# Kernel optimization log

Hardware: AMD Instinct MI355X
Metric: run time of the kernel (lower is better)

Reference implementation:

```python
import jax, jax.numpy as jnp
import numpy as np

B, H, S, D = 2, 16, 2048, 64


def setup_inputs() -> dict:
    key = jax.random.key(0)
    kq, kk, kv = jax.random.split(key, 3)
    queries = jax.random.normal(kq, (B, H, S, D), dtype=jnp.float32)
    keys = jax.random.normal(kk, (B, H, S, D), dtype=jnp.float32)
    values = jax.random.normal(kv, (B, H, S, D), dtype=jnp.float32)
    # causal mask: True = attend, False = masked (matches masked_fill(mask == 0, -inf))
    mask = jnp.tril(jnp.ones((S, S), dtype=bool))[None, None, :, :]
    return {"queries": queries, "keys": keys, "values": values, "mask": mask}


def reference(queries, keys, values, mask):
    d_k = queries.shape[-1]
    scale = 1.0 / jnp.sqrt(jnp.asarray(d_k, dtype=queries.dtype))
    # scores: [B,H,S,S]
    scores = jnp.einsum("bhqd,bhkd->bhqk", queries, keys) * scale
    scores = jnp.where(mask, scores, -jnp.inf)
    attention = jax.nn.softmax(scores, axis=-1)
    # dropout p=0.0 (eval-mode reference) -> identity
    return jnp.einsum("bhqk,bhkd->bhqd", attention, values)
```

## Files before the change

kernel.cpp:

```cpp
#include <hip/hip_runtime.h>
#include <hip/hip_bf16.h>

#define S_LEN 2048
#define D_DIM 64
#define KVB   64
#define QS    (0.125f * 1.44269504088896341f)

using f32x4  = __attribute__((ext_vector_type(4))) float;
using bf16x8 = __attribute__((ext_vector_type(8))) short;

__device__ __forceinline__ unsigned short f2bf(float f) {
    return __builtin_bit_cast(unsigned short, __float2bfloat16(f));
}
__device__ __forceinline__ unsigned pk2bf(float lo, float hi) {
    return (unsigned)f2bf(lo) | ((unsigned)f2bf(hi) << 16);
}
__device__ __forceinline__ int swz(int r, int c) {
    return (r * 64 + c) ^ ((r & 7) << 3);
}

template<int C>
__device__ __forceinline__ float dppf(float x) {
    return __builtin_bit_cast(float,
        __builtin_amdgcn_mov_dpp(__builtin_bit_cast(int, x), C, 0xf, 0xf, true));
}
__device__ __forceinline__ float red16_max(float v) {
    v = fmaxf(v, dppf<0xB1>(v));
    v = fmaxf(v, dppf<0x4E>(v));
    v = fmaxf(v, dppf<0x141>(v));
    v = fmaxf(v, dppf<0x140>(v));
    return v;
}
__device__ __forceinline__ float red16_sum(float v) {
    v += dppf<0xB1>(v);
    v += dppf<0x4E>(v);
    v += dppf<0x141>(v);
    v += dppf<0x140>(v);
    return v;
}

__global__ __launch_bounds__(256, 4)
void attn_fwd(const float* __restrict__ Qg, const float* __restrict__ Kg,
              const float* __restrict__ Vg, float* __restrict__ Og) {
    __shared__ __align__(16) unsigned short lds[20480];

    const int wg = blockIdx.x;
    const int x  = wg & 7;
    const int s  = (wg >> 3) & 31;
    const int r  = wg >> 8;
    const int bh = x * 4 + r;
    const int q  = (r & 1) ? (31 - s) : s;

    const int tid  = threadIdx.x;
    const int wid  = tid >> 6;
    const int lane = tid & 63;
    const int lo   = lane & 15;
    const int hi   = lane >> 4;

    const size_t boff = (size_t)bh * (S_LEN * D_DIM);
    const float* Qp = Qg + boff;
    const float* Kp = Kg + boff;
    const float* Vp = Vg + boff;
    float*       Op = Og + boff;

    const int qrow0 = q * 64 + wid * 16;

    bf16x8 qf[2];
    #pragma unroll
    for (int kc = 0; kc < 2; ++kc) {
        const float* src = Qp + (size_t)(qrow0 + lo) * D_DIM + kc * 32 + hi * 8;
        f32x4 a = *(const f32x4*)src;
        f32x4 b = *(const f32x4*)(src + 4);
        union { bf16x8 v; unsigned u[4]; } fr;
        fr.u[0] = pk2bf(a[0] * QS, a[1] * QS);
        fr.u[1] = pk2bf(a[2] * QS, a[3] * QS);
        fr.u[2] = pk2bf(b[0] * QS, b[1] * QS);
        fr.u[3] = pk2bf(b[2] * QS, b[3] * QS);
        qf[kc] = fr.v;
    }

    float mrow[4], lrow[4];
    f32x4 oacc[4];
    #pragma unroll
    for (int rr = 0; rr < 4; ++rr) { mrow[rr] = -INFINITY; lrow[rr] = 0.f; }
    #pragma unroll
    for (int dn = 0; dn < 4; ++dn) oacc[dn] = f32x4{0.f, 0.f, 0.f, 0.f};

    const int kr    = tid >> 2;
    const int kcb   = (tid & 3) << 4;
    const int vr    = (tid & 31) << 1;
    const int vcb   = (tid >> 5) << 3;
    const int pbase = 16384 + (wid << 10);

    const int T = q + 1;
    f32x4 kst[4], vst[4];

    {
        const float* ks = Kp + (size_t)kr * D_DIM + kcb;
        kst[0] = *(const f32x4*)ks;       kst[1] = *(const f32x4*)(ks + 4);
        kst[2] = *(const f32x4*)(ks + 8); kst[3] = *(const f32x4*)(ks + 12);
        const float* vs = Vp + (size_t)vr * D_DIM + vcb;
        vst[0] = *(const f32x4*)vs;           vst[1] = *(const f32x4*)(vs + 4);
        vst[2] = *(const f32x4*)(vs + D_DIM); vst[3] = *(const f32x4*)(vs + D_DIM + 4);
        union { uint4 w4; unsigned u[4]; } w;
        w.u[0] = pk2bf(kst[0][0], kst[0][1]); w.u[1] = pk2bf(kst[0][2], kst[0][3]);
        w.u[2] = pk2bf(kst[1][0], kst[1][1]); w.u[3] = pk2bf(kst[1][2], kst[1][3]);
        *(uint4*)&lds[swz(kr, kcb)] = w.w4;
        w.u[0] = pk2bf(kst[2][0], kst[2][1]); w.u[1] = pk2bf(kst[2][2], kst[2][3]);
        w.u[2] = pk2bf(kst[3][0], kst[3][1]); w.u[3] = pk2bf(kst[3][2], kst[3][3]);
        *(uint4*)&lds[swz(kr, kcb + 8)] = w.w4;
        #pragma unroll
        for (int c = 0; c < 8; ++c) {
            unsigned pv = pk2bf(vst[c >> 2][c & 3], vst[2 + (c >> 2)][c & 3]);
            *(unsigned*)&lds[4096 + swz(vcb + c, vr)] = pv;
        }
    }
    __syncthreads();

    for (int t = 0; t < T; ++t) {
        const int kA = (t & 1) << 13;
        const int vA = kA + 4096;
        const bool pf = (t + 1 < T);

        if (pf) {
            const int nb = (t + 1) * KVB;
            const float* ks = Kp + (size_t)(nb + kr) * D_DIM + kcb;
            kst[0] = *(const f32x4*)ks;       kst[1] = *(const f32x4*)(ks + 4);
            kst[2] = *(const f32x4*)(ks + 8); kst[3] = *(const f32x4*)(ks + 12);
            const float* vs = Vp + (size_t)(nb + vr) * D_DIM + vcb;
            vst[0] = *(const f32x4*)vs;           vst[1] = *(const f32x4*)(vs + 4);
            vst[2] = *(const f32x4*)(vs + D_DIM); vst[3] = *(const f32x4*)(vs + D_DIM + 4);
        }

        f32x4 sc[4];
        __builtin_amdgcn_s_setprio(1);
        #pragma unroll
        for (int nt = 0; nt < 4; ++nt) {
            f32x4 acc = f32x4{0.f, 0.f, 0.f, 0.f};
            #pragma unroll
            for (int kc = 0; kc < 2; ++kc) {
                bf16x8 kf = *(const bf16x8*)&lds[kA + swz(nt * 16 + lo, kc * 32 + hi * 8)];
                acc = __builtin_amdgcn_mfma_f32_16x16x32_bf16(qf[kc], kf, acc, 0, 0, 0);
            }
            sc[nt] = acc;
        }
        __builtin_amdgcn_s_setprio(0);
        if (t == q) {
            const int kb = t * KVB;
            #pragma unroll
            for (int nt = 0; nt < 4; ++nt)
                #pragma unroll
                for (int rr = 0; rr < 4; ++rr)
                    if (kb + nt * 16 + lo > qrow0 + hi * 4 + rr) sc[nt][rr] = -INFINITY;
        }
        float pm[4];
        #pragma unroll
        for (int rr = 0; rr < 4; ++rr)
            pm[rr] = red16_max(fmaxf(fmaxf(sc[0][rr], sc[1][rr]), fmaxf(sc[2][rr], sc[3][rr])));

        bool resc = false;
        #pragma unroll
        for (int rr = 0; rr < 4; ++rr) resc |= (pm[rr] > mrow[rr] + 8.f);
        if (__any(resc)) {
            #pragma unroll
            for (int rr = 0; rr < 4; ++rr) {
                const float mn = fmaxf(mrow[rr], pm[rr]);
                const float al = __builtin_amdgcn_exp2f(mrow[rr] - mn);
                mrow[rr] = mn;
                lrow[rr] *= al;
                #pragma unroll
                for (int dn = 0; dn < 4; ++dn) oacc[dn][rr] *= al;
            }
        }
        float rs[4] = {0.f, 0.f, 0.f, 0.f};
        #pragma unroll
        for (int nt = 0; nt < 4; ++nt)
            #pragma unroll
            for (int rr = 0; rr < 4; ++rr) {
                float p = __builtin_amdgcn_exp2f(sc[nt][rr] - mrow[rr]);
                rs[rr] += p;
                lds[pbase + swz(hi * 4 + rr, nt * 16 + lo)] = f2bf(p);
            }
        #pragma unroll
        for (int rr = 0; rr < 4; ++rr) lrow[rr] += red16_sum(rs[rr]);

        __builtin_amdgcn_s_setprio(1);
        #pragma unroll
        for (int dn = 0; dn < 4; ++dn)
            #pragma unroll
            for (int kc = 0; kc < 2; ++kc) {
                bf16x8 pfr = *(const bf16x8*)&lds[pbase + swz(lo, kc * 32 + hi * 8)];
                bf16x8 vfr = *(const bf16x8*)&lds[vA + swz(dn * 16 + lo, kc * 32 + hi * 8)];
                oacc[dn] = __builtin_amdgcn_mfma_f32_16x16x32_bf16(pfr, vfr, oacc[dn], 0, 0, 0);
            }
        __builtin_amdgcn_s_setprio(0);

        if (pf) {
            const int nA = ((t + 1) & 1) << 13;
            union { uint4 w4; unsigned u[4]; } w;
            w.u[0] = pk2bf(kst[0][0], kst[0][1]); w.u[1] = pk2bf(kst[0][2], kst[0][3]);
            w.u[2] = pk2bf(kst[1][0], kst[1][1]); w.u[3] = pk2bf(kst[1][2], kst[1][3]);
            *(uint4*)&lds[nA + swz(kr, kcb)] = w.w4;
            w.u[0] = pk2bf(kst[2][0], kst[2][1]); w.u[1] = pk2bf(kst[2][2], kst[2][3]);
            w.u[2] = pk2bf(kst[3][0], kst[3][1]); w.u[3] = pk2bf(kst[3][2], kst[3][3]);
            *(uint4*)&lds[nA + swz(kr, kcb + 8)] = w.w4;
            #pragma unroll
            for (int c = 0; c < 8; ++c) {
                unsigned pv = pk2bf(vst[c >> 2][c & 3], vst[2 + (c >> 2)][c & 3]);
                *(unsigned*)&lds[nA + 4096 + swz(vcb + c, vr)] = pv;
            }
        }
        __syncthreads();
    }

    #pragma unroll
    for (int rr = 0; rr < 4; ++rr) {
        const float inv = 1.0f / lrow[rr];
        #pragma unroll
        for (int dn = 0; dn < 4; ++dn)
            Op[(size_t)(qrow0 + hi * 4 + rr) * D_DIM + dn * 16 + lo] = oacc[dn][rr] * inv;
    }
}

extern "C" void kernel_launch(void* const* d_in, const int* in_sizes, int n_in,
                              void* d_out, int out_size, void* d_ws, size_t ws_size,
                              hipStream_t stream) {
    const float* Q = (const float*)d_in[0];
    const float* K = (const float*)d_in[1];
    const float* V = (const float*)d_in[2];
    float* O = (float*)d_out;
    attn_fwd<<<dim3(32 * 32), dim3(256), 0, stream>>>(Q, K, V, O);
}
```

Baseline: 166.2 us.

## Pre-convert K/V to swizzled bf16 workspace and stage via global_load_lds

Adds two prep kernels that convert K to bf16 and V to transposed bf16, each already in the swizzled LDS tile layout, and write them to the workspace. The attention kernel then copies each tile straight from global memory into LDS with global_load_lds, so the per-iteration fp32 loads, conversions and LDS stores are gone, along with about half the bytes read per tile. The cost is two extra launches and an extra round trip of K/V through memory. The old kernel is kept as a fallback when the workspace is too small.

Result: faster. 151.0 us (-9.1%).

```diff
diff --git a/kernel.cpp b/kernel.cpp
--- a/kernel.cpp
+++ b/kernel.cpp
@@ -39,9 +39,57 @@
     return v;
 }
 
+typedef const __attribute__((address_space(1))) unsigned short* gas_p;
+typedef __attribute__((address_space(3))) unsigned short*       las_p;
+__device__ __forceinline__ void stage16(const unsigned short* g, unsigned short* l) {
+    __builtin_amdgcn_global_load_lds((gas_p)g, (las_p)l, 16, 0, 0);
+}
+
+__global__ __launch_bounds__(256)
+void prep_k(const float* __restrict__ Kg, unsigned short* __restrict__ wsK) {
+    const int base = (blockIdx.x * 256 + threadIdx.x) * 8;
+    const int bh   = base >> 17;
+    const int rem  = base & 131071;
+    const int r    = rem >> 6;
+    const int c0   = rem & 63;
+    f32x4 a = *(const f32x4*)(Kg + base);
+    f32x4 b = *(const f32x4*)(Kg + base + 4);
+    union { uint4 w4; unsigned u[4]; } w;
+    w.u[0] = pk2bf(a[0], a[1]); w.u[1] = pk2bf(a[2], a[3]);
+    w.u[2] = pk2bf(b[0], b[1]); w.u[3] = pk2bf(b[2], b[3]);
+    *(uint4*)&wsK[bh * 131072 + (r >> 6) * 4096 + swz(r & 63, c0)] = w.w4;
+}
+
+__global__ __launch_bounds__(256)
+void prep_v(const float* __restrict__ Vg, unsigned short* __restrict__ wsV) {
+    __shared__ float ldsF[64 * 68];
+    const int bh  = blockIdx.x >> 5;
+    const int t   = blockIdx.x & 31;
+    const int tid = threadIdx.x;
+    const int kvr = tid >> 2;
+    const int c0  = (tid & 3) << 4;
+    const float* src = Vg + (size_t)bh * 131072 + (size_t)(t * 64 + kvr) * 64 + c0;
+    #pragma unroll
+    for (int j = 0; j < 4; ++j)
+        *(f32x4*)&ldsF[kvr * 68 + c0 + j * 4] = *(const f32x4*)(src + j * 4);
+    __syncthreads();
+    #pragma unroll
+    for (int i = 0; i < 2; ++i) {
+        const int d   = tid & 63;
+        const int kv0 = ((tid >> 6) << 3) + (i << 5);
+        float p[8];
+        #pragma unroll
+        for (int j = 0; j < 8; ++j) p[j] = ldsF[(kv0 + j) * 68 + d];
+        union { uint4 w4; unsigned u[4]; } w;
+        w.u[0] = pk2bf(p[0], p[1]); w.u[1] = pk2bf(p[2], p[3]);
+        w.u[2] = pk2bf(p[4], p[5]); w.u[3] = pk2bf(p[6], p[7]);
+        *(uint4*)&wsV[bh * 131072 + t * 4096 + swz(d, kv0)] = w.w4;
+    }
+}
+
 __global__ __launch_bounds__(256, 4)
-void attn_fwd(const float* __restrict__ Qg, const float* __restrict__ Kg,
-              const float* __restrict__ Vg, float* __restrict__ Og) {
+void attn_fast(const float* __restrict__ Qg, const unsigned short* __restrict__ wsK,
+               const unsigned short* __restrict__ wsV, float* __restrict__ Og) {
     __shared__ __align__(16) unsigned short lds[20480];
 
     const int wg = blockIdx.x;
@@ -57,11 +105,10 @@
     const int lo   = lane & 15;
     const int hi   = lane >> 4;
 
-    const size_t boff = (size_t)bh * (S_LEN * D_DIM);
-    const float* Qp = Qg + boff;
-    const float* Kp = Kg + boff;
-    const float* Vp = Vg + boff;
-    float*       Op = Og + boff;
+    const float* Qp = Qg + (size_t)bh * (S_LEN * D_DIM);
+    float*       Op = Og + (size_t)bh * (S_LEN * D_DIM);
+    const unsigned short* kws = wsK + (size_t)bh * 131072;
+    const unsigned short* vws = wsV + (size_t)bh * 131072;
 
     const int qrow0 = q * 64 + wid * 16;
 
@@ -86,15 +133,155 @@
     #pragma unroll
     for (int dn = 0; dn < 4; ++dn) oacc[dn] = f32x4{0.f, 0.f, 0.f, 0.f};
 
+    const int pbase = 16384 + (wid << 10);
+    const int T = q + 1;
+
+    #pragma unroll
+    for (int j = 0; j < 2; ++j) {
+        const int so = (wid * 2 + j) * 512;
+        stage16(kws + so + lane * 8, &lds[so]);
+        stage16(vws + so + lane * 8, &lds[4096 + so]);
+    }
+    __syncthreads();
+
+    for (int t = 0; t < T; ++t) {
+        const int kA = (t & 1) << 13;
+        const int vA = kA + 4096;
+        const bool pf = (t + 1 < T);
+
+        if (pf) {
+            const int nA = ((t + 1) & 1) << 13;
+            const int tb = (t + 1) * 4096;
+            #pragma unroll
+            for (int j = 0; j < 2; ++j) {
+                const int so = (wid * 2 + j) * 512;
+                stage16(kws + tb + so + lane * 8, &lds[nA + so]);
+                stage16(vws + tb + so + lane * 8, &lds[nA + 4096 + so]);
+            }
+        }
+
+        f32x4 sc[4];
+        __builtin_amdgcn_s_setprio(1);
+        #pragma unroll
+        for (int nt = 0; nt < 4; ++nt) {
+            f32x4 acc = f32x4{0.f, 0.f, 0.f, 0.f};
+            #pragma unroll
+            for (int kc = 0; kc < 2; ++kc) {
+                bf16x8 kf = *(const bf16x8*)&lds[kA + swz(nt * 16 + lo, kc * 32 + hi * 8)];
+                acc = __builtin_amdgcn_mfma_f32_16x16x32_bf16(qf[kc], kf, acc, 0, 0, 0);
+            }
+            sc[nt] = acc;
+        }
+        __builtin_amdgcn_s_setprio(0);
+        if (t == q) {
+            const int kb = t * KVB;
+            #pragma unroll
+            for (int nt = 0; nt < 4; ++nt)
+                #pragma unroll
+                for (int rr = 0; rr < 4; ++rr)
+                    if (kb + nt * 16 + lo > qrow0 + hi * 4 + rr) sc[nt][rr] = -INFINITY;
+        }
+        float pm[4];
+        #pragma unroll
+        for (int rr = 0; rr < 4; ++rr)
+            pm[rr] = red16_max(fmaxf(fmaxf(sc[0][rr], sc[1][rr]), fmaxf(sc[2][rr], sc[3][rr])));
+
+        bool resc = false;
+        #pragma unroll
+        for (int rr = 0; rr < 4; ++rr) resc |= (pm[rr] > mrow[rr] + 8.f);
+        if (__any(resc)) {
+            #pragma unroll
+            for (int rr = 0; rr < 4; ++rr) {
+                const float mn = fmaxf(mrow[rr], pm[rr]);
+                const float al = __builtin_amdgcn_exp2f(mrow[rr] - mn);
+                mrow[rr] = mn;
+                lrow[rr] *= al;
+                #pragma unroll
+                for (int dn = 0; dn < 4; ++dn) oacc[dn][rr] *= al;
+            }
+        }
+        float rs[4] = {0.f, 0.f, 0.f, 0.f};
+        #pragma unroll
+        for (int nt = 0; nt < 4; ++nt)
+            #pragma unroll
+            for (int rr = 0; rr < 4; ++rr) {
+                float p = __builtin_amdgcn_exp2f(sc[nt][rr] - mrow[rr]);
+                rs[rr] += p;
+                lds[pbase + swz(hi * 4 + rr, nt * 16 + lo)] = f2bf(p);
+            }
+        #pragma unroll
+        for (int rr = 0; rr < 4; ++rr) lrow[rr] += red16_sum(rs[rr]);
+
+        __builtin_amdgcn_s_setprio(1);
+        #pragma unroll
+        for (int dn = 0; dn < 4; ++dn)
+            #pragma unroll
+            for (int kc = 0; kc < 2; ++kc) {
+                bf16x8 pfr = *(const bf16x8*)&lds[pbase + swz(lo, kc * 32 + hi * 8)];
+                bf16x8 vfr = *(const bf16x8*)&lds[vA + swz(dn * 16 + lo, kc * 32 + hi * 8)];
+                oacc[dn] = __builtin_amdgcn_mfma_f32_16x16x32_bf16(pfr, vfr, oacc[dn], 0, 0, 0);
+            }
+        __builtin_amdgcn_s_setprio(0);
+
+        __syncthreads();
+    }
+
+    #pragma unroll
+    for (int rr = 0; rr < 4; ++rr) {
+        const float inv = 1.0f / lrow[rr];
+        #pragma unroll
+        for (int dn = 0; dn < 4; ++dn)
+            Op[(size_t)(qrow0 + hi * 4 + rr) * D_DIM + dn * 16 + lo] = oacc[dn][rr] * inv;
+    }
+}
+
+__global__ __launch_bounds__(256, 4)
+void attn_fb(const float* __restrict__ Qg, const float* __restrict__ Kg,
+             const float* __restrict__ Vg, float* __restrict__ Og) {
+    __shared__ __align__(16) unsigned short lds[20480];
+    const int wg = blockIdx.x;
+    const int x  = wg & 7;
+    const int s  = (wg >> 3) & 31;
+    const int r  = wg >> 8;
+    const int bh = x * 4 + r;
+    const int q  = (r & 1) ? (31 - s) : s;
+    const int tid  = threadIdx.x;
+    const int wid  = tid >> 6;
+    const int lane = tid & 63;
+    const int lo   = lane & 15;
+    const int hi   = lane >> 4;
+    const size_t boff = (size_t)bh * (S_LEN * D_DIM);
+    const float* Qp = Qg + boff;
+    const float* Kp = Kg + boff;
+    const float* Vp = Vg + boff;
+    float*       Op = Og + boff;
+    const int qrow0 = q * 64 + wid * 16;
+    bf16x8 qf[2];
+    #pragma unroll
+    for (int kc = 0; kc < 2; ++kc) {
+        const float* src = Qp + (size_t)(qrow0 + lo) * D_DIM + kc * 32 + hi * 8;
+        f32x4 a = *(const f32x4*)src;
+        f32x4 b = *(const f32x4*)(src + 4);
+        union { bf16x8 v; unsigned u[4]; } fr;
+        fr.u[0] = pk2bf(a[0] * QS, a[1] * QS);
+        fr.u[1] = pk2bf(a[2] * QS, a[3] * QS);
+        fr.u[2] = pk2bf(b[0] * QS, b[1] * QS);
+        fr.u[3] = pk2bf(b[2] * QS, b[3] * QS);
+        qf[kc] = fr.v;
+    }
+    float mrow[4], lrow[4];
+    f32x4 oacc[4];
+    #pragma unroll
+    for (int rr = 0; rr < 4; ++rr) { mrow[rr] = -INFINITY; lrow[rr] = 0.f; }
+    #pragma unroll
+    for (int dn = 0; dn < 4; ++dn) oacc[dn] = f32x4{0.f, 0.f, 0.f, 0.f};
     const int kr    = tid >> 2;
     const int kcb   = (tid & 3) << 4;
     const int vr    = (tid & 31) << 1;
     const int vcb   = (tid >> 5) << 3;
     const int pbase = 16384 + (wid << 10);
-
     const int T = q + 1;
     f32x4 kst[4], vst[4];
-
     {
         const float* ks = Kp + (size_t)kr * D_DIM + kcb;
         kst[0] = *(const f32x4*)ks;       kst[1] = *(const f32x4*)(ks + 4);
@@ -116,12 +303,10 @@
         }
     }
     __syncthreads();
-
     for (int t = 0; t < T; ++t) {
         const int kA = (t & 1) << 13;
         const int vA = kA + 4096;
         const bool pf = (t + 1 < T);
-
         if (pf) {
             const int nb = (t + 1) * KVB;
             const float* ks = Kp + (size_t)(nb + kr) * D_DIM + kcb;
@@ -131,7 +316,6 @@
             vst[0] = *(const f32x4*)vs;           vst[1] = *(const f32x4*)(vs + 4);
             vst[2] = *(const f32x4*)(vs + D_DIM); vst[3] = *(const f32x4*)(vs + D_DIM + 4);
         }
-
         f32x4 sc[4];
         __builtin_amdgcn_s_setprio(1);
         #pragma unroll
@@ -157,7 +341,6 @@
         #pragma unroll
         for (int rr = 0; rr < 4; ++rr)
             pm[rr] = red16_max(fmaxf(fmaxf(sc[0][rr], sc[1][rr]), fmaxf(sc[2][rr], sc[3][rr])));
-
         bool resc = false;
         #pragma unroll
         for (int rr = 0; rr < 4; ++rr) resc |= (pm[rr] > mrow[rr] + 8.f);
@@ -183,7 +366,6 @@
             }
         #pragma unroll
         for (int rr = 0; rr < 4; ++rr) lrow[rr] += red16_sum(rs[rr]);
-
         __builtin_amdgcn_s_setprio(1);
         #pragma unroll
         for (int dn = 0; dn < 4; ++dn)
@@ -194,7 +376,6 @@
                 oacc[dn] = __builtin_amdgcn_mfma_f32_16x16x32_bf16(pfr, vfr, oacc[dn], 0, 0, 0);
             }
         __builtin_amdgcn_s_setprio(0);
-
         if (pf) {
             const int nA = ((t + 1) & 1) << 13;
             union { uint4 w4; unsigned u[4]; } w;
@@ -212,7 +393,6 @@
         }
         __syncthreads();
     }
-
     #pragma unroll
     for (int rr = 0; rr < 4; ++rr) {
         const float inv = 1.0f / lrow[rr];
@@ -229,5 +409,14 @@
     const float* K = (const float*)d_in[1];
     const float* V = (const float*)d_in[2];
     float* O = (float*)d_out;
-    attn_fwd<<<dim3(32 * 32), dim3(256), 0, stream>>>(Q, K, V, O);
-}
+    const size_t wsNeed = (size_t)32 * 131072 * 2 * sizeof(unsigned short);
+    if (ws_size >= wsNeed) {
+        unsigned short* wsK = (unsigned short*)d_ws;
+        unsigned short* wsV = wsK + (size_t)32 * 131072;
+        prep_k<<<dim3(2048), dim3(256), 0, stream>>>(K, wsK);
+        prep_v<<<dim3(1024), dim3(256), 0, stream>>>(V, wsV);
+        attn_fast<<<dim3(1024), dim3(256), 0, stream>>>(Q, wsK, wsV, O);
+    } else {
+        attn_fb<<<dim3(1024), dim3(256), 0, stream>>>(Q, K, V, O);
+    }
+}
```
